# Optimization experiments

Measured on AMD Instinct MI355X. Metric: run time of the kernel, lower is better.

Reference implementation:

```python
import jax, jax.numpy as jnp
import numpy as np

TOP_K_FRACTION = 0.1


def setup_inputs() -> dict:
    key = jax.random.key(0)
    k1, k2, k3 = jax.random.split(key, 3)
    B, H, S, D = 2, 12, 1024, 64
    q = jax.random.normal(k1, (B, H, S, D), dtype=jnp.float32)
    k = jax.random.normal(k2, (B, H, S, D), dtype=jnp.float32)
    v = jax.random.normal(k3, (B, H, S, D), dtype=jnp.float32)
    mask = jnp.zeros((B, 1, 1, S), dtype=jnp.float32)
    return {"q": q, "k": k, "v": v, "mask": mask}


def reference(q, k, v, mask):
    B, H, S, D = q.shape
    k_precise = max(1, int(S * TOP_K_FRACTION))
    # binary (sign) approximation of attention scores; detached like torch
    q_bin = jnp.sign(jax.lax.stop_gradient(q))
    k_bin = jnp.sign(jax.lax.stop_gradient(k))
    approx_scores = jnp.einsum('bhsd,bhtd->bhst', q_bin, k_bin) / D  # [B,H,S,S]
    _, topk_idx = jax.lax.top_k(approx_scores, k_precise)  # [B,H,S,kp]
    # gather top-k keys/values per query: [B,H,S,kp,D]
    k_gathered = jnp.take_along_axis(k[:, :, None, :, :], topk_idx[..., None], axis=3)
    v_gathered = jnp.take_along_axis(v[:, :, None, :, :], topk_idx[..., None], axis=3)
    scale = np.float32(1.0 / np.sqrt(D))
    precise_scores = jnp.einsum('bhsd,bhskd->bhsk', q, k_gathered) * scale
    # gather mask along key positions: mask [B,1,1,S] -> [B,H,S,kp]
    mask_gathered = jnp.take_along_axis(
        jnp.broadcast_to(mask, (B, H, S, S)), topk_idx, axis=-1)
    precise_scores = precise_scores + mask_gathered
    precise_probs = jax.nn.softmax(precise_scores, axis=-1)
    attn_output = jnp.einsum('bhsk,bhskd->bhsd', precise_probs, v_gathered)
    return attn_output
```

## Files before the change

kernel.cpp:

```cpp
#include <hip/hip_runtime.h>
#include <hip/hip_fp16.h>
#include <cstdint>

#define BB 2
#define HH 12
#define SS 1024
#define DD 64
#define KP 102
#define KPAD 104
#define QPB 4

typedef _Float16 half2v __attribute__((ext_vector_type(2)));
typedef _Float16 half8v __attribute__((ext_vector_type(8)));

template <int CTRL>
__device__ __forceinline__ float dpp_f(float x) {
    return __builtin_bit_cast(float,
        __builtin_amdgcn_update_dpp(0, __builtin_bit_cast(int, x), CTRL, 0xF, 0xF, false));
}
__device__ __forceinline__ float group8_sum(float x) {
    x += dpp_f<0xB1>(x);
    x += dpp_f<0x4E>(x);
    x += dpp_f<0x141>(x);
    return x;
}
__device__ __forceinline__ int mbcnt64(unsigned long long m) {
    return (int)__builtin_amdgcn_mbcnt_hi((unsigned)(m >> 32),
               __builtin_amdgcn_mbcnt_lo((unsigned)(m & 0xffffffffull), 0u));
}
__device__ __forceinline__ half2v shfl_xor_h2(half2v v, int m) {
    return __builtin_bit_cast(half2v, __shfl_xor(__builtin_bit_cast(int, v), m));
}

__global__ __launch_bounds__(256) void pack_kernel(
    const float* __restrict__ k, const float* __restrict__ v,
    unsigned long long* __restrict__ kbits, _Float16* __restrict__ kvh)
{
    int row  = (int)((blockIdx.x * 256 + threadIdx.x) >> 6);
    int lane = (int)(threadIdx.x & 63);
    if (row >= BB * HH * SS) return;
    float kv = k[(size_t)row * DD + lane];
    float vv = v[(size_t)row * DD + lane];
    unsigned long long km = __ballot(kv > 0.0f);
    kvh[(size_t)row * 128 + lane]      = (_Float16)kv;
    kvh[(size_t)row * 128 + 64 + lane] = (_Float16)vv;
    if (lane == 0) kbits[row] = km;
}

__global__ __launch_bounds__(256, 4) void battn_kernel(
    const float* __restrict__ q, const _Float16* __restrict__ kvh,
    const float* __restrict__ mask,
    const unsigned long long* __restrict__ kbits,
    float* __restrict__ out)
{
    const int tid  = (int)threadIdx.x;
    const int w    = tid >> 6;
    const int lane = tid & 63;
    const int query = (int)blockIdx.x * QPB + w;
    const int bh    = query >> 10;
    const int b     = bh / HH;

    __shared__ int sel_t[QPB][KPAD];

    const float qreg = q[(size_t)query * DD + lane];
    const unsigned long long qm = __ballot(qreg > 0.0f);

    const unsigned long long* kb = kbits + (size_t)bh * SS;
    int pbin[16];
    #pragma unroll
    for (int j = 0; j < 16; ++j)
        pbin[j] = (int)__popcll(qm ^ kb[j * 64 + lane]);

    #define COUNT_LE(P, OUTC)                                      \
        { int _c = 0;                                              \
          _Pragma("unroll")                                        \
          for (int j = 0; j < 16; ++j)                             \
              _c += (int)__popcll(__ballot(pbin[j] <= (P)));       \
          (OUTC) = _c; }
    int P = 27, c, clt;
    COUNT_LE(P, c);
    if (c >= KP) {
        COUNT_LE(P - 1, clt);
        while (clt >= KP) { c = clt; --P; COUNT_LE(P - 1, clt); }
    } else {
        do { clt = c; ++P; COUNT_LE(P, c); } while (c < KP);
    }
    const int binP = P;
    const int need = KP - clt;
    #undef COUNT_LE

    if (lane < KPAD - KP)
        sel_t[w][KP + lane] = 0;
    int base = 0, tie_base = 0;
    #pragma unroll
    for (int j = 0; j < 16; ++j) {
        bool isGt  = pbin[j] < binP;
        bool isTie = (pbin[j] == binP);
        unsigned long long tiem = __ballot(isTie);
        int rank = tie_base + mbcnt64(tiem);
        bool take = isGt || (isTie && rank < need);
        unsigned long long tm = __ballot(take);
        if (take)
            sel_t[w][base + mbcnt64(tm)] = j * 64 + lane;
        base     += (int)__popcll(tm);
        tie_base += (int)__popcll(tiem);
    }

    const int sub = lane & 7, g = lane >> 3;
    const float* qrow = q + (size_t)query * DD + sub * 8;
    half2v qh[4];
    #pragma unroll
    for (int d = 0; d < 4; ++d) {
        float2 f2 = *(const float2*)(qrow + d * 2);
        half2v h; h[0] = (_Float16)(f2.x * 0.125f); h[1] = (_Float16)(f2.y * 0.125f);
        qh[d] = h;
    }
    const _Float16* kvrows  = kvh + (size_t)bh * SS * 128;
    const float*    maskrow = mask + (size_t)b * SS;

    half2v acch[4];
    #pragma unroll
    for (int d = 0; d < 4; ++d) { acch[d][0] = (_Float16)0; acch[d][1] = (_Float16)0; }
    float l_part = 0.0f;

    #pragma unroll
    for (int ii = 0; ii < 13; ++ii) {
        const int i = ii * 8 + g;
        const int t = sel_t[w][i];
        const _Float16* p = kvrows + (size_t)t * 128 + sub * 8;
        half8v kv8 = *(const half8v*)p;
        half8v vv8 = *(const half8v*)(p + 64);
        half2v k0; k0[0] = kv8[0]; k0[1] = kv8[1];
        half2v k1; k1[0] = kv8[2]; k1[1] = kv8[3];
        half2v k2; k2[0] = kv8[4]; k2[1] = kv8[5];
        half2v k3; k3[0] = kv8[6]; k3[1] = kv8[7];
        float s = fmaf(maskrow[t], 0.125f, -0.5f);
        s = __builtin_amdgcn_fdot2(qh[0], k0, s, false);
        s = __builtin_amdgcn_fdot2(qh[1], k1, s, false);
        s = __builtin_amdgcn_fdot2(qh[2], k2, s, false);
        s = __builtin_amdgcn_fdot2(qh[3], k3, s, false);
        s = group8_sum(s);
        float e = __expf(s);
        if (ii == 12 && i >= KP) e = 0.0f;
        l_part += e;
        _Float16 eh = (_Float16)e;
        half2v e2; e2[0] = eh; e2[1] = eh;
        #pragma unroll
        for (int d = 0; d < 4; ++d) {
            half2v v2; v2[0] = vv8[d * 2]; v2[1] = vv8[d * 2 + 1];
            acch[d] = e2 * v2 + acch[d];
        }
    }

    float l = l_part;
    l += __shfl_xor(l, 8);
    l += __shfl_xor(l, 16);
    l += __shfl_xor(l, 32);
    #pragma unroll
    for (int d = 0; d < 4; ++d) {
        acch[d] = acch[d] + shfl_xor_h2(acch[d], 8);
        acch[d] = acch[d] + shfl_xor_h2(acch[d], 16);
        acch[d] = acch[d] + shfl_xor_h2(acch[d], 32);
    }
    if (lane < 8) {
        const float rinv = __frcp_rn(l);
        float* orow = out + (size_t)query * DD + lane * 8;
        float4 o0 = make_float4((float)acch[0][0] * rinv, (float)acch[0][1] * rinv,
                                (float)acch[1][0] * rinv, (float)acch[1][1] * rinv);
        float4 o1 = make_float4((float)acch[2][0] * rinv, (float)acch[2][1] * rinv,
                                (float)acch[3][0] * rinv, (float)acch[3][1] * rinv);
        *(float4*)orow       = o0;
        *(float4*)(orow + 4) = o1;
    }
}

extern "C" void kernel_launch(void* const* d_in, const int* in_sizes, int n_in,
                              void* d_out, int out_size, void* d_ws, size_t ws_size,
                              hipStream_t stream) {
    const float* q    = (const float*)d_in[0];
    const float* k    = (const float*)d_in[1];
    const float* v    = (const float*)d_in[2];
    const float* mask = (const float*)d_in[3];
    float* out = (float*)d_out;

    const int rows = BB * HH * SS;
    unsigned long long* kbits = (unsigned long long*)d_ws;
    _Float16* kvh = (_Float16*)((char*)d_ws + (size_t)rows * sizeof(unsigned long long));

    pack_kernel<<<(rows * 64 + 255) / 256, 256, 0, stream>>>(k, v, kbits, kvh);
    battn_kernel<<<rows / QPB, 256, 0, stream>>>(q, kvh, mask, kbits, out);
}
```

Before: 110.0 us.

## Replace sparse gather attention with dense MFMA attention masked by top-k bitmask

Splits the kernel into a selection pass that writes a per-query 1024-bit selection mask and a dense attention pass that computes all 1024 scores per query with 16x16x32 f16 MFMA instructions, zeroing the non-selected probabilities via the mask. V is pre-transposed to fp16 in a new kernel so the PV product can also use MFMA, and K is prescaled during packing. This trades roughly ten times more arithmetic for coalesced, contiguous loads and matrix-core throughput in place of scattered per-key gathers. It also adds two extra launches, workspace traffic for the mask and transposed V, and a cross-wave LDS reduction.

```diff
diff --git a/kernel.cpp b/kernel.cpp
--- a/kernel.cpp
+++ b/kernel.cpp
@@ -7,60 +7,63 @@
 #define SS 1024
 #define DD 64
 #define KP 102
-#define KPAD 104
 #define QPB 4
 
 typedef _Float16 half2v __attribute__((ext_vector_type(2)));
 typedef _Float16 half8v __attribute__((ext_vector_type(8)));
-
-template <int CTRL>
-__device__ __forceinline__ float dpp_f(float x) {
-    return __builtin_bit_cast(float,
-        __builtin_amdgcn_update_dpp(0, __builtin_bit_cast(int, x), CTRL, 0xF, 0xF, false));
-}
-__device__ __forceinline__ float group8_sum(float x) {
-    x += dpp_f<0xB1>(x);
-    x += dpp_f<0x4E>(x);
-    x += dpp_f<0x141>(x);
-    return x;
-}
+typedef float    f32x4  __attribute__((ext_vector_type(4)));
+
 __device__ __forceinline__ int mbcnt64(unsigned long long m) {
     return (int)__builtin_amdgcn_mbcnt_hi((unsigned)(m >> 32),
                __builtin_amdgcn_mbcnt_lo((unsigned)(m & 0xffffffffull), 0u));
 }
-__device__ __forceinline__ half2v shfl_xor_h2(half2v v, int m) {
-    return __builtin_bit_cast(half2v, __shfl_xor(__builtin_bit_cast(int, v), m));
-}
 
 __global__ __launch_bounds__(256) void pack_kernel(
-    const float* __restrict__ k, const float* __restrict__ v,
-    unsigned long long* __restrict__ kbits, _Float16* __restrict__ kvh)
+    const float* __restrict__ k,
+    unsigned long long* __restrict__ kbits, _Float16* __restrict__ kh)
 {
     int row  = (int)((blockIdx.x * 256 + threadIdx.x) >> 6);
     int lane = (int)(threadIdx.x & 63);
     if (row >= BB * HH * SS) return;
     float kv = k[(size_t)row * DD + lane];
-    float vv = v[(size_t)row * DD + lane];
     unsigned long long km = __ballot(kv > 0.0f);
-    kvh[(size_t)row * 128 + lane]      = (_Float16)kv;
-    kvh[(size_t)row * 128 + 64 + lane] = (_Float16)vv;
+    kh[(size_t)row * DD + lane] = (_Float16)(kv * 0.125f);
     if (lane == 0) kbits[row] = km;
 }
 
-__global__ __launch_bounds__(256, 4) void battn_kernel(
-    const float* __restrict__ q, const _Float16* __restrict__ kvh,
-    const float* __restrict__ mask,
+__global__ __launch_bounds__(256) void vtrans_kernel(
+    const float* __restrict__ v, _Float16* __restrict__ vT)
+{
+    __shared__ _Float16 lds[64][66];
+    const int t = (int)threadIdx.x;
+    const int kb64 = (int)blockIdx.x * 64;
+    const int bh = kb64 >> 10;
+    const int keybase = kb64 & (SS - 1);
+    #pragma unroll
+    for (int e = 0; e < 16; ++e) {
+        int key = e * 4 + (t >> 6);
+        int dim = t & 63;
+        lds[key][dim] = (_Float16)v[((size_t)kb64 + key) * DD + dim];
+    }
+    __syncthreads();
+    #pragma unroll
+    for (int e = 0; e < 16; ++e) {
+        int dim = e * 4 + (t >> 6);
+        int key = t & 63;
+        vT[((size_t)bh * DD + dim) * SS + keybase + key] = lds[key][dim];
+    }
+}
+
+__global__ __launch_bounds__(256, 4) void select_kernel(
+    const float* __restrict__ q,
     const unsigned long long* __restrict__ kbits,
-    float* __restrict__ out)
+    unsigned long long* __restrict__ selmask)
 {
     const int tid  = (int)threadIdx.x;
     const int w    = tid >> 6;
     const int lane = tid & 63;
     const int query = (int)blockIdx.x * QPB + w;
     const int bh    = query >> 10;
-    const int b     = bh / HH;
-
-    __shared__ int sel_t[QPB][KPAD];
 
     const float qreg = q[(size_t)query * DD + lane];
     const unsigned long long qm = __ballot(qreg > 0.0f);
@@ -89,9 +92,8 @@
     const int need = KP - clt;
     #undef COUNT_LE
 
-    if (lane < KPAD - KP)
-        sel_t[w][KP + lane] = 0;
-    int base = 0, tie_base = 0;
+    unsigned long long* selq = selmask + (size_t)query * 16;
+    int tie_base = 0;
     #pragma unroll
     for (int j = 0; j < 16; ++j) {
         bool isGt  = pbin[j] < binP;
@@ -100,77 +102,127 @@
         int rank = tie_base + mbcnt64(tiem);
         bool take = isGt || (isTie && rank < need);
         unsigned long long tm = __ballot(take);
-        if (take)
-            sel_t[w][base + mbcnt64(tm)] = j * 64 + lane;
-        base     += (int)__popcll(tm);
+        if (lane == 0) selq[j] = tm;
         tie_base += (int)__popcll(tiem);
     }
-
-    const int sub = lane & 7, g = lane >> 3;
-    const float* qrow = q + (size_t)query * DD + sub * 8;
-    half2v qh[4];
-    #pragma unroll
-    for (int d = 0; d < 4; ++d) {
-        float2 f2 = *(const float2*)(qrow + d * 2);
-        half2v h; h[0] = (_Float16)(f2.x * 0.125f); h[1] = (_Float16)(f2.y * 0.125f);
-        qh[d] = h;
-    }
-    const _Float16* kvrows  = kvh + (size_t)bh * SS * 128;
-    const float*    maskrow = mask + (size_t)b * SS;
-
-    half2v acch[4];
-    #pragma unroll
-    for (int d = 0; d < 4; ++d) { acch[d][0] = (_Float16)0; acch[d][1] = (_Float16)0; }
+}
+
+__global__ __launch_bounds__(256, 4) void attn_kernel(
+    const float* __restrict__ q, const _Float16* __restrict__ kh,
+    const _Float16* __restrict__ vT, const float* __restrict__ mask,
+    const unsigned long long* __restrict__ selmask,
+    float* __restrict__ out)
+{
+    const int tid  = (int)threadIdx.x;
+    const int w    = tid >> 6;
+    const int lane = tid & 63;
+    const int r    = lane & 15;
+    const int g    = lane >> 4;
+    const int qbase = (int)blockIdx.x * 16;
+    const int bh = qbase >> 10;
+    const int b  = bh / HH;
+    const int query = qbase + r;
+
+    __shared__ _Float16 pbuf[4][16][40];
+    __shared__ float    mbuf[4][64][17];
+
+    half8v qf[2];
+    #pragma unroll
+    for (int mb = 0; mb < 2; ++mb) {
+        const float* qp = q + (size_t)query * DD + mb * 32 + g * 8;
+        float4 f0 = *(const float4*)qp;
+        float4 f1 = *(const float4*)(qp + 4);
+        half8v h;
+        h[0] = (_Float16)f0.x; h[1] = (_Float16)f0.y;
+        h[2] = (_Float16)f0.z; h[3] = (_Float16)f0.w;
+        h[4] = (_Float16)f1.x; h[5] = (_Float16)f1.y;
+        h[6] = (_Float16)f1.z; h[7] = (_Float16)f1.w;
+        qf[mb] = h;
+    }
+
+    const unsigned* selp = (const unsigned*)(selmask + (size_t)query * 16 + w * 4);
+    uint4 sm0 = *(const uint4*)selp;
+    uint4 sm1 = *(const uint4*)(selp + 4);
+    unsigned smw[8] = {sm0.x, sm0.y, sm0.z, sm0.w, sm1.x, sm1.y, sm1.z, sm1.w};
+
+    const _Float16* khb   = kh + ((size_t)bh * SS + w * 256) * DD;
+    const _Float16* vTb   = vT + (size_t)bh * DD * SS + w * 256;
+    const float*    maskb = mask + (size_t)b * SS + w * 256;
+
+    f32x4 oacc[4];
+    #pragma unroll
+    for (int db = 0; db < 4; ++db) oacc[db] = (f32x4){0.f, 0.f, 0.f, 0.f};
     float l_part = 0.0f;
-
-    #pragma unroll
-    for (int ii = 0; ii < 13; ++ii) {
-        const int i = ii * 8 + g;
-        const int t = sel_t[w][i];
-        const _Float16* p = kvrows + (size_t)t * 128 + sub * 8;
-        half8v kv8 = *(const half8v*)p;
-        half8v vv8 = *(const half8v*)(p + 64);
-        half2v k0; k0[0] = kv8[0]; k0[1] = kv8[1];
-        half2v k1; k1[0] = kv8[2]; k1[1] = kv8[3];
-        half2v k2; k2[0] = kv8[4]; k2[1] = kv8[5];
-        half2v k3; k3[0] = kv8[6]; k3[1] = kv8[7];
-        float s = fmaf(maskrow[t], 0.125f, -0.5f);
-        s = __builtin_amdgcn_fdot2(qh[0], k0, s, false);
-        s = __builtin_amdgcn_fdot2(qh[1], k1, s, false);
-        s = __builtin_amdgcn_fdot2(qh[2], k2, s, false);
-        s = __builtin_amdgcn_fdot2(qh[3], k3, s, false);
-        s = group8_sum(s);
-        float e = __expf(s);
-        if (ii == 12 && i >= KP) e = 0.0f;
-        l_part += e;
-        _Float16 eh = (_Float16)e;
-        half2v e2; e2[0] = eh; e2[1] = eh;
-        #pragma unroll
-        for (int d = 0; d < 4; ++d) {
-            half2v v2; v2[0] = vv8[d * 2]; v2[1] = vv8[d * 2 + 1];
-            acch[d] = e2 * v2 + acch[d];
-        }
-    }
-
-    float l = l_part;
-    l += __shfl_xor(l, 8);
-    l += __shfl_xor(l, 16);
-    l += __shfl_xor(l, 32);
-    #pragma unroll
-    for (int d = 0; d < 4; ++d) {
-        acch[d] = acch[d] + shfl_xor_h2(acch[d], 8);
-        acch[d] = acch[d] + shfl_xor_h2(acch[d], 16);
-        acch[d] = acch[d] + shfl_xor_h2(acch[d], 32);
-    }
-    if (lane < 8) {
-        const float rinv = __frcp_rn(l);
-        float* orow = out + (size_t)query * DD + lane * 8;
-        float4 o0 = make_float4((float)acch[0][0] * rinv, (float)acch[0][1] * rinv,
-                                (float)acch[1][0] * rinv, (float)acch[1][1] * rinv);
-        float4 o1 = make_float4((float)acch[2][0] * rinv, (float)acch[2][1] * rinv,
-                                (float)acch[3][0] * rinv, (float)acch[3][1] * rinv);
-        *(float4*)orow       = o0;
-        *(float4*)(orow + 4) = o1;
+    const int g4 = g * 4, g8 = g * 8;
+
+    #pragma unroll
+    for (int kc = 0; kc < 8; ++kc) {
+        f32x4 ct[2];
+        #pragma unroll
+        for (int tt = 0; tt < 2; ++tt) {
+            const _Float16* kp = khb + (size_t)(kc * 32 + tt * 16 + r) * DD + g8;
+            half8v ka0 = *(const half8v*)kp;
+            half8v ka1 = *(const half8v*)(kp + 32);
+            f32x4 cacc = (f32x4){0.f, 0.f, 0.f, 0.f};
+            cacc = __builtin_amdgcn_mfma_f32_16x16x32_f16(ka0, qf[0], cacc, 0, 0, 0);
+            cacc = __builtin_amdgcn_mfma_f32_16x16x32_f16(ka1, qf[1], cacc, 0, 0, 0);
+            ct[tt] = cacc;
+        }
+        const unsigned sw = smw[kc];
+        #pragma unroll
+        for (int tt = 0; tt < 2; ++tt) {
+            float4 mv = *(const float4*)(maskb + kc * 32 + tt * 16 + g4);
+            float mvj[4] = {mv.x, mv.y, mv.z, mv.w};
+            float e[4];
+            #pragma unroll
+            for (int j = 0; j < 4; ++j) {
+                float s  = ct[tt][j] + mvj[j];
+                float ev = __expf(s);
+                unsigned bit = (sw >> (tt * 16 + g4 + j)) & 1u;
+                ev = bit ? ev : 0.0f;
+                e[j] = ev;
+                l_part += ev;
+            }
+            half2v p0; p0[0] = (_Float16)e[0]; p0[1] = (_Float16)e[1];
+            half2v p1; p1[0] = (_Float16)e[2]; p1[1] = (_Float16)e[3];
+            *(half2v*)&pbuf[w][r][tt * 16 + g4]     = p0;
+            *(half2v*)&pbuf[w][r][tt * 16 + g4 + 2] = p1;
+        }
+        half8v pf = *(const half8v*)&pbuf[w][r][g8];
+        #pragma unroll
+        for (int db = 0; db < 4; ++db) {
+            const _Float16* vp = vTb + (size_t)(db * 16 + r) * SS + kc * 32 + g8;
+            half8v va = *(const half8v*)vp;
+            oacc[db] = __builtin_amdgcn_mfma_f32_16x16x32_f16(va, pf, oacc[db], 0, 0, 0);
+        }
+    }
+
+    l_part += __shfl_xor(l_part, 16);
+    l_part += __shfl_xor(l_part, 32);
+
+    #pragma unroll
+    for (int db = 0; db < 4; ++db)
+        #pragma unroll
+        for (int j = 0; j < 4; ++j)
+            mbuf[w][lane][db * 4 + j] = oacc[db][j];
+    mbuf[w][lane][16] = l_part;
+    __syncthreads();
+
+    {
+        const int row = tid & 15, gg = (tid >> 4) & 3, db = tid >> 6;
+        const int src = gg * 16 + row;
+        float o0 = 0.f, o1 = 0.f, o2 = 0.f, o3 = 0.f, ls = 0.f;
+        #pragma unroll
+        for (int ww = 0; ww < 4; ++ww) {
+            o0 += mbuf[ww][src][db * 4 + 0];
+            o1 += mbuf[ww][src][db * 4 + 1];
+            o2 += mbuf[ww][src][db * 4 + 2];
+            o3 += mbuf[ww][src][db * 4 + 3];
+            ls += mbuf[ww][src][16];
+        }
+        const float rinv = __frcp_rn(ls);
+        float4 o = make_float4(o0 * rinv, o1 * rinv, o2 * rinv, o3 * rinv);
+        *(float4*)(out + (size_t)(qbase + row) * DD + db * 16 + gg * 4) = o;
     }
 }
 
@@ -184,9 +236,16 @@
     float* out = (float*)d_out;
 
     const int rows = BB * HH * SS;
-    unsigned long long* kbits = (unsigned long long*)d_ws;
-    _Float16* kvh = (_Float16*)((char*)d_ws + (size_t)rows * sizeof(unsigned long long));
-
-    pack_kernel<<<(rows * 64 + 255) / 256, 256, 0, stream>>>(k, v, kbits, kvh);
-    battn_kernel<<<rows / QPB, 256, 0, stream>>>(q, kvh, mask, kbits, out);
-}
+    char* ws = (char*)d_ws;
+    unsigned long long* kbits = (unsigned long long*)ws;
+    _Float16* kh = (_Float16*)(ws + (size_t)rows * 8);
+    _Float16* vT = (_Float16*)(ws + (size_t)rows * 8
+                                  + (size_t)rows * DD * 2);
+    unsigned long long* selmask = (unsigned long long*)(ws + (size_t)rows * 8
+                                  + 2 * (size_t)rows * DD * 2);
+
+    pack_kernel<<<(rows * 64 + 255) / 256, 256, 0, stream>>>(k, kbits, kh);
+    vtrans_kernel<<<rows / 64, 256, 0, stream>>>(v, vT);
+    select_kernel<<<rows / QPB, 256, 0, stream>>>(q, kbits, selmask);
+    attn_kernel<<<rows / 16, 256, 0, stream>>>(q, kh, vT, mask, selmask, out);
+}
```

After: 148.3 us. 34.9% more time.
